# Kernel tuning notes

Measured on AMD Instinct MI355X. Metric: run time of the kernel, lower is better.

## Reference

```python
import jax, jax.numpy as jnp
import numpy as np

DIM = 1024
NUM_HEADS = 16
HEAD_DIM = DIM // NUM_HEADS
SCALE = 1.0 / float(np.sqrt(HEAD_DIM))


def setup_inputs() -> dict:
    key = jax.random.key(0)
    ks = jax.random.split(key, 8)
    b, n = 1, 4096
    x = jax.random.normal(ks[0], (b, n, DIM), dtype=jnp.float32)
    cos = jax.random.uniform(ks[1], (b, n, HEAD_DIM // 2), dtype=jnp.float32)
    sin = jax.random.uniform(ks[2], (b, n, HEAD_DIM // 2), dtype=jnp.float32)
    # qkv Linear(dim, 3*dim) and proj Linear(dim, dim); store weights as [in, out]
    w_qkv = jax.random.normal(ks[3], (DIM, 3 * DIM), dtype=jnp.float32) * (1.0 / np.sqrt(DIM))
    b_qkv = jax.random.normal(ks[4], (3 * DIM,), dtype=jnp.float32) * 0.01
    w_proj = jax.random.normal(ks[5], (DIM, DIM), dtype=jnp.float32) * (1.0 / np.sqrt(DIM))
    b_proj = jax.random.normal(ks[6], (DIM,), dtype=jnp.float32) * 0.01
    return {"x": x, "cos": cos, "sin": sin, "w_qkv": w_qkv, "b_qkv": b_qkv,
            "w_proj": w_proj, "b_proj": b_proj}


def _rotate_half(t):
    t1, t2 = jnp.split(t, 2, axis=-1)
    return jnp.concatenate([-t2, t1], axis=-1)


def reference(x, cos, sin, w_qkv, b_qkv, w_proj, b_proj):
    b, n, d = x.shape
    qkv = x @ w_qkv + b_qkv                      # [b, n, 3d]
    q, k, v = jnp.split(qkv, 3, axis=-1)
    # [b, n, h, hd] layout (avoids explicit transposes; einsum handles head axis)
    q = q.reshape(b, n, NUM_HEADS, HEAD_DIM)
    k = k.reshape(b, n, NUM_HEADS, HEAD_DIM)
    v = v.reshape(b, n, NUM_HEADS, HEAD_DIM)
    # RoPE: cos/sin [b, n, hd/2] -> [b, n, 1, hd], broadcast over heads
    cos_f = jnp.concatenate([cos, cos], axis=-1)[:, :, None, :]
    sin_f = jnp.concatenate([sin, sin], axis=-1)[:, :, None, :]
    q = q * cos_f + _rotate_half(q) * sin_f
    k = k * cos_f + _rotate_half(k) * sin_f
    # SDPA (non-causal, no dropout in eval)
    scores = jnp.einsum("bqhd,bkhd->bhqk", q, k) * SCALE
    attn = jax.nn.softmax(scores, axis=-1)
    out = jnp.einsum("bhqk,bkhd->bqhd", attn, v).reshape(b, n, d)
    return out @ w_proj + b_proj
```

## Files before the change

kernel.cpp:

```cpp
#include <hip/hip_runtime.h>
#include <hip/hip_bf16.h>
#include <cstdint>


#define TOK 4096
#define DIM_ 1024
#define NHEAD 16
#define HDIM 64
#define N3 3072
#define SCALE_LOG2E 0.18033688011112042f

typedef __bf16 bf16_t;
typedef bf16_t bf16x8 __attribute__((ext_vector_type(8)));
typedef float floatx4 __attribute__((ext_vector_type(4)));

__device__ __forceinline__ void async_ld16(const bf16_t* g, bf16_t* l) {
  __builtin_amdgcn_global_load_lds(
      (const __attribute__((address_space(1))) void*)(g),
      (__attribute__((address_space(3))) void*)(l), 16, 0, 0);
}

__global__ __launch_bounds__(256) void k_prep(
    const float* __restrict__ x, const float* __restrict__ w_qkv,
    const float* __restrict__ w_proj, bf16_t* __restrict__ xb,
    bf16_t* __restrict__ wqkvT, bf16_t* __restrict__ wprojT) {
  __shared__ float tile[32][33];
  const int b = blockIdx.x;
  if (b < 4096) {
    int i = b * 256 + threadIdx.x;
    float4 v = ((const float4*)x)[i];
    union { bf16_t bb[4]; uint64_t u; } p;
    p.bb[0] = (bf16_t)v.x; p.bb[1] = (bf16_t)v.y;
    p.bb[2] = (bf16_t)v.z; p.bb[3] = (bf16_t)v.w;
    ((uint64_t*)xb)[i] = p.u;
    return;
  }
  const float* in; bf16_t* out; int R, C, c0, r0;
  if (b < 7168) {
    int bb = b - 4096; in = w_qkv; out = wqkvT; R = 1024; C = 3072;
    c0 = (bb % 96) * 32; r0 = (bb / 96) * 32;
  } else {
    int bb = b - 7168; in = w_proj; out = wprojT; R = 1024; C = 1024;
    c0 = (bb % 32) * 32; r0 = (bb / 32) * 32;
  }
  int tx = threadIdx.x & 31, ty = threadIdx.x >> 5;
#pragma unroll
  for (int i = 0; i < 4; i++) {
    int r = ty + i * 8;
    tile[r][tx] = in[(size_t)(r0 + r) * C + c0 + tx];
  }
  __syncthreads();
#pragma unroll
  for (int i = 0; i < 4; i++) {
    int c = ty + i * 8;
    out[(size_t)(c0 + c) * R + r0 + tx] = (bf16_t)tile[tx][c];
  }
}

__global__ __launch_bounds__(256) void k_qkv(
    const bf16_t* __restrict__ A,
    const bf16_t* __restrict__ Bt,
    const float* __restrict__ bias,
    const float* __restrict__ cs,
    const float* __restrict__ sn,
    bf16_t* __restrict__ qb, bf16_t* __restrict__ kb, bf16_t* __restrict__ vT) {
  constexpr int K = 1024, BK = 32;
  __shared__ bf16_t As[128 * BK] __attribute__((aligned(16)));
  __shared__ bf16_t Bs[128 * BK] __attribute__((aligned(16)));
  const int t = threadIdx.x;
  const int lane = t & 63, w = t >> 6;
  const int lrow = lane & 15, quad = lane >> 4;
  const int m0 = blockIdx.y * 128, n0 = blockIdx.x * 128;
  const int wm = (w >> 1) * 64, wn = (w & 1) * 64;

  const floatx4 ZV = {0.f, 0.f, 0.f, 0.f};
  floatx4 acc[4][4];
#pragma unroll
  for (int i = 0; i < 4; i++)
#pragma unroll
    for (int j = 0; j < 4; j++) acc[i][j] = ZV;

  for (int kt = 0; kt < K; kt += BK) {
#pragma unroll
    for (int r = 0; r < 2; r++) {
      int idx = r * 256 + t;
      int lbase = (r * 256 + w * 64) * 8;
      async_ld16(&A[(size_t)(m0 + (idx >> 2)) * K + kt + (idx & 3) * 8], &As[lbase]);
      async_ld16(&Bt[(size_t)(n0 + (idx >> 2)) * K + kt + (idx & 3) * 8], &Bs[lbase]);
    }
    __syncthreads();
    bf16x8 af[4], bf[4];
#pragma unroll
    for (int i = 0; i < 4; i++)
      af[i] = *(const bf16x8*)&As[(wm + i * 16 + lrow) * BK + quad * 8];
#pragma unroll
    for (int i = 0; i < 4; i++)
      bf[i] = *(const bf16x8*)&Bs[(wn + i * 16 + lrow) * BK + quad * 8];
#pragma unroll
    for (int mi = 0; mi < 4; mi++)
#pragma unroll
      for (int ni = 0; ni < 4; ni++)
        acc[mi][ni] = __builtin_amdgcn_mfma_f32_16x16x32_bf16(af[mi], bf[ni], acc[mi][ni], 0, 0, 0);
    __syncthreads();
  }

  const int c0 = n0 + wn;
  const int seg = c0 >> 10;
  const int h = (c0 & 1023) >> 6;
  float bv[4];
#pragma unroll
  for (int ni = 0; ni < 4; ni++) bv[ni] = bias[c0 + ni * 16 + lrow];

  if (seg < 2) {
    bf16_t* base = ((seg == 0) ? qb : kb) + (size_t)h * TOK * HDIM;
    const float qs = (seg == 0) ? SCALE_LOG2E : 1.0f;
#pragma unroll
    for (int mi = 0; mi < 4; mi++) {
#pragma unroll
      for (int reg = 0; reg < 4; reg++) {
        const int r = m0 + wm + mi * 16 + quad * 4 + reg;
        const float c_lo = cs[r * 32 + lrow];
        const float c_hi = cs[r * 32 + 16 + lrow];
        const float s_lo = sn[r * 32 + lrow];
        const float s_hi = sn[r * 32 + 16 + lrow];
        const float v0 = acc[mi][0][reg] + bv[0];
        const float v1 = acc[mi][1][reg] + bv[1];
        const float v2 = acc[mi][2][reg] + bv[2];
        const float v3 = acc[mi][3][reg] + bv[3];
        const float o0 = (v0 * c_lo - v2 * s_lo) * qs;
        const float o1 = (v1 * c_hi - v3 * s_hi) * qs;
        const float o2 = (v2 * c_lo + v0 * s_lo) * qs;
        const float o3 = (v3 * c_hi + v1 * s_hi) * qs;
        bf16_t* rp = base + (size_t)r * HDIM + lrow;
        rp[0]  = (bf16_t)o0;
        rp[16] = (bf16_t)o1;
        rp[32] = (bf16_t)o2;
        rp[48] = (bf16_t)o3;
      }
    }
  } else {
    bf16_t* base = vT + (size_t)h * HDIM * TOK;
#pragma unroll
    for (int mi = 0; mi < 4; mi++) {
      const int rbase = m0 + wm + mi * 16 + quad * 4;
#pragma unroll
      for (int ni = 0; ni < 4; ni++) {
        union { bf16_t b[4]; uint64_t u; } p;
#pragma unroll
        for (int reg = 0; reg < 4; reg++) p.b[reg] = (bf16_t)(acc[mi][ni][reg] + bv[ni]);
        *(uint64_t*)&base[(size_t)(ni * 16 + lrow) * TOK + rbase] = p.u;
      }
    }
  }
}

__global__ __launch_bounds__(256, 2) void k_attn(
    const bf16_t* __restrict__ qb, const bf16_t* __restrict__ kb,
    const bf16_t* __restrict__ vT, bf16_t* __restrict__ ao) {
  __shared__ bf16_t Ks[2][64 * 64] __attribute__((aligned(16)));
  __shared__ bf16_t Vs[2][64 * 64] __attribute__((aligned(16)));
  __shared__ bf16_t Ps[4][64 * 36] __attribute__((aligned(16)));
  const int t = threadIdx.x, lane = t & 63, w = t >> 6;
  const int lrow = lane & 15, quad = lane >> 4;
  const int qg = w & 1, kh = w >> 1;
  const int h = blockIdx.x & 15;
  const int q0 = (blockIdx.x >> 4) * 128;
  const bf16_t* qh = qb + (size_t)h * TOK * HDIM;
  const bf16_t* khp = kb + (size_t)h * TOK * HDIM;
  const bf16_t* vhp = vT + (size_t)h * HDIM * TOK;
  bf16_t* Pw = &Ps[w][0];

  const int ksrc = (t >> 3) * HDIM + (((t & 7) ^ ((t >> 3) & 7)) * 8);
  const int vsrc = (t >> 3) * TOK + (((t & 7) ^ ((t >> 3) & 7)) * 8);

  bf16x8 qf[4][2];
#pragma unroll
  for (int ni = 0; ni < 4; ni++)
#pragma unroll
    for (int ks = 0; ks < 2; ks++)
      qf[ni][ks] = *(const bf16x8*)&qh[(size_t)(q0 + qg * 64 + ni * 16 + lrow) * HDIM + ks * 32 + quad * 8];

  const floatx4 ZV = {0.f, 0.f, 0.f, 0.f};
  floatx4 o[4][4];
  floatx4 lacc[4] = {ZV, ZV, ZV, ZV};
#pragma unroll
  for (int d = 0; d < 4; d++)
#pragma unroll
    for (int ni = 0; ni < 4; ni++) o[d][ni] = ZV;

#pragma unroll
  for (int r = 0; r < 2; r++) {
    async_ld16(&khp[(size_t)(r * 32) * HDIM + ksrc], &Ks[0][r * 2048 + t * 8]);
    async_ld16(&vhp[(size_t)(r * 32) * TOK + vsrc], &Vs[0][r * 2048 + t * 8]);
  }

  for (int it = 0; it < TOK / 64; ++it) {
    const int b = it & 1;
    __syncthreads();
    if (it + 1 < TOK / 64) {
      const int j1 = (it + 1) * 64;
#pragma unroll
      for (int r = 0; r < 2; r++) {
        async_ld16(&khp[((size_t)j1 + r * 32) * HDIM + ksrc], &Ks[b ^ 1][r * 2048 + t * 8]);
        async_ld16(&vhp[(size_t)(r * 32) * TOK + j1 + vsrc], &Vs[b ^ 1][r * 2048 + t * 8]);
      }
    }

    floatx4 s[2][4];
#pragma unroll
    for (int mi = 0; mi < 2; mi++)
#pragma unroll
      for (int ni = 0; ni < 4; ni++) s[mi][ni] = ZV;
#pragma unroll
    for (int ks = 0; ks < 2; ks++)
#pragma unroll
      for (int mi = 0; mi < 2; mi++) {
        bf16x8 kf = *(const bf16x8*)&Ks[b][(kh * 32 + mi * 16 + lrow) * 64 + (((ks * 4 + quad) ^ (lrow & 7)) * 8)];
#pragma unroll
        for (int ni = 0; ni < 4; ni++)
          s[mi][ni] = __builtin_amdgcn_mfma_f32_16x16x32_bf16(kf, qf[ni][ks], s[mi][ni], 0, 0, 0);
      }

#pragma unroll
    for (int mi = 0; mi < 2; mi++)
#pragma unroll
      for (int ni = 0; ni < 4; ni++) {
#pragma unroll
        for (int reg = 0; reg < 4; reg++)
          s[mi][ni][reg] = __builtin_amdgcn_exp2f(s[mi][ni][reg]);
        lacc[ni] += s[mi][ni];
      }

#pragma unroll
    for (int mi = 0; mi < 2; mi++)
#pragma unroll
      for (int ni = 0; ni < 4; ni++) {
        union { bf16_t b4[4]; uint64_t u; } p;
#pragma unroll
        for (int reg = 0; reg < 4; reg++) p.b4[reg] = (bf16_t)s[mi][ni][reg];
        *(uint64_t*)&Pw[(ni * 16 + lrow) * 36 + (mi * 4 + quad) * 4] = p.u;
      }

    bf16x8 pf[4];
#pragma unroll
    for (int ni = 0; ni < 4; ni++) {
      const int row = (ni * 16 + lrow) * 36;
      union { uint64_t u[2]; bf16x8 v; } pp;
      pp.u[0] = *(const uint64_t*)&Pw[row + quad * 8];
      pp.u[1] = *(const uint64_t*)&Pw[row + quad * 8 + 4];
      pf[ni] = pp.v;
    }
#pragma unroll
    for (int dt = 0; dt < 4; dt++) {
      bf16x8 vf = *(const bf16x8*)&Vs[b][(dt * 16 + lrow) * 64 + (((kh * 4 + quad) ^ (lrow & 7)) * 8)];
#pragma unroll
      for (int ni = 0; ni < 4; ni++)
        o[dt][ni] = __builtin_amdgcn_mfma_f32_16x16x32_bf16(vf, pf[ni], o[dt][ni], 0, 0, 0);
    }
  }

  __syncthreads();
  float* Mrg = (qg == 0) ? (float*)&Ks[0][0] : (float*)&Vs[0][0];
  float* Lmrg = (float*)&Ps[0][0];
  float lq[4];
#pragma unroll
  for (int ni = 0; ni < 4; ni++) {
    float l = lacc[ni][0] + lacc[ni][1] + lacc[ni][2] + lacc[ni][3];
    l += __shfl_xor(l, 16, 64);
    l += __shfl_xor(l, 32, 64);
    lq[ni] = l;
  }
  if (kh == 1) {
#pragma unroll
    for (int ni = 0; ni < 4; ni++) {
#pragma unroll
      for (int dt = 0; dt < 4; dt++)
        *(floatx4*)&Mrg[(ni * 16 + lrow) * 64 + dt * 16 + quad * 4] = o[dt][ni];
      if (quad == 0) Lmrg[qg * 64 + ni * 16 + lrow] = lq[ni];
    }
  }
  __syncthreads();
  if (kh == 0) {
#pragma unroll
    for (int ni = 0; ni < 4; ni++) {
      const float l = lq[ni] + Lmrg[qg * 64 + ni * 16 + lrow];
      const float inv = 1.0f / l;
      const int qrow = q0 + qg * 64 + ni * 16 + lrow;
#pragma unroll
      for (int dt = 0; dt < 4; dt++) {
        floatx4 ov = *(const floatx4*)&Mrg[(ni * 16 + lrow) * 64 + dt * 16 + quad * 4];
        union { bf16_t b4[4]; uint64_t u; } p;
#pragma unroll
        for (int reg = 0; reg < 4; reg++) p.b4[reg] = (bf16_t)((o[dt][ni][reg] + ov[reg]) * inv);
        *(uint64_t*)&ao[(size_t)qrow * DIM_ + h * HDIM + dt * 16 + quad * 4] = p.u;
      }
    }
  }
}

__global__ __launch_bounds__(256) void k_proj(
    const bf16_t* __restrict__ A,
    const bf16_t* __restrict__ Bt,
    const float* __restrict__ bias, float* __restrict__ out) {
  constexpr int K = 1024, BK = 32;
  __shared__ bf16_t As[64 * BK] __attribute__((aligned(16)));
  __shared__ bf16_t Bs[128 * BK] __attribute__((aligned(16)));
  const int t = threadIdx.x;
  const int lane = t & 63, w = t >> 6;
  const int lrow = lane & 15, quad = lane >> 4;
  const int m0 = blockIdx.y * 64, n0 = blockIdx.x * 128;
  const int wm = (w >> 1) * 32, wn = (w & 1) * 64;

  const floatx4 ZV = {0.f, 0.f, 0.f, 0.f};
  floatx4 acc[2][4];
#pragma unroll
  for (int i = 0; i < 2; i++)
#pragma unroll
    for (int j = 0; j < 4; j++) acc[i][j] = ZV;

  for (int kt = 0; kt < K; kt += BK) {
    async_ld16(&A[(size_t)(m0 + (t >> 2)) * K + kt + (t & 3) * 8], &As[w * 512]);
#pragma unroll
    for (int r = 0; r < 2; r++) {
      int idx = r * 256 + t;
      async_ld16(&Bt[(size_t)(n0 + (idx >> 2)) * K + kt + (idx & 3) * 8],
                 &Bs[(r * 256 + w * 64) * 8]);
    }
    __syncthreads();
    bf16x8 af[2], bf[4];
#pragma unroll
    for (int i = 0; i < 2; i++)
      af[i] = *(const bf16x8*)&As[(wm + i * 16 + lrow) * BK + quad * 8];
#pragma unroll
    for (int i = 0; i < 4; i++)
      bf[i] = *(const bf16x8*)&Bs[(wn + i * 16 + lrow) * BK + quad * 8];
#pragma unroll
    for (int mi = 0; mi < 2; mi++)
#pragma unroll
      for (int ni = 0; ni < 4; ni++)
        acc[mi][ni] = __builtin_amdgcn_mfma_f32_16x16x32_bf16(af[mi], bf[ni], acc[mi][ni], 0, 0, 0);
    __syncthreads();
  }

  const int c0 = n0 + wn;
#pragma unroll
  for (int ni = 0; ni < 4; ni++) {
    float bv = bias[c0 + ni * 16 + lrow];
#pragma unroll
    for (int mi = 0; mi < 2; mi++)
#pragma unroll
      for (int reg = 0; reg < 4; reg++) {
        int r = m0 + wm + mi * 16 + quad * 4 + reg;
        out[(size_t)r * DIM_ + c0 + ni * 16 + lrow] = acc[mi][ni][reg] + bv;
      }
  }
}

extern "C" void kernel_launch(void* const* d_in, const int* in_sizes, int n_in,
                              void* d_out, int out_size, void* d_ws, size_t ws_size,
                              hipStream_t stream) {
  const float* x      = (const float*)d_in[0];
  const float* cs     = (const float*)d_in[1];
  const float* sn     = (const float*)d_in[2];
  const float* w_qkv  = (const float*)d_in[3];
  const float* b_qkv  = (const float*)d_in[4];
  const float* w_proj = (const float*)d_in[5];
  const float* b_proj = (const float*)d_in[6];
  float* out = (float*)d_out;

  char* ws = (char*)d_ws;
  bf16_t* xb     = (bf16_t*)(ws);
  bf16_t* wqkvT  = (bf16_t*)(ws + 8388608);
  bf16_t* wprojT = (bf16_t*)(ws + 14680064);
  bf16_t* qb     = (bf16_t*)(ws + 16777216);
  bf16_t* kb     = (bf16_t*)(ws + 25165824);
  bf16_t* vT     = (bf16_t*)(ws + 33554432);
  bf16_t* ao     = xb;

  k_prep<<<dim3(8192), dim3(256), 0, stream>>>(x, w_qkv, w_proj, xb, wqkvT, wprojT);
  k_qkv<<<dim3(24, 32), dim3(256), 0, stream>>>(xb, wqkvT, b_qkv, cs, sn, qb, kb, vT);
  k_attn<<<dim3(512), dim3(256), 0, stream>>>(qb, kb, vT, ao);
  k_proj<<<dim3(8, 64), dim3(256), 0, stream>>>(ao, wprojT, b_proj, out);
}
```

Before: 222.2 us.

## Switch attention to 32x32x16 MFMA and keep P in registers

The attention kernel now uses 32x32x16 bf16 MFMAs instead of 16x16x32. The S accumulator layout then lines up with the B-operand layout the PV MFMA needs, so the exponentiated P tile is packed to bf16 in registers and the per-wave LDS round trip through Ps is dropped. V fragments are read from LDS as two 8-byte halves matching the permuted key order, and the final merge keeps only a small Lm array. This removes LDS traffic and LDS footprint, at the cost of larger accumulators (floatx16) and possible register pressure under launch_bounds(256,2).

Result: slower. 232.4 us (+4.6%).

```diff
diff --git a/kernel.cpp b/kernel.cpp
--- a/kernel.cpp
+++ b/kernel.cpp
@@ -13,11 +13,18 @@
 typedef __bf16 bf16_t;
 typedef bf16_t bf16x8 __attribute__((ext_vector_type(8)));
 typedef float floatx4 __attribute__((ext_vector_type(4)));
+typedef float floatx16 __attribute__((ext_vector_type(16)));
 
 __device__ __forceinline__ void async_ld16(const bf16_t* g, bf16_t* l) {
   __builtin_amdgcn_global_load_lds(
       (const __attribute__((address_space(1))) void*)(g),
       (__attribute__((address_space(3))) void*)(l), 16, 0, 0);
+}
+
+__device__ __forceinline__ uint32_t pkbf(float a, float b) {
+  union { bf16_t h[2]; uint32_t u; } x;
+  x.h[0] = (bf16_t)a; x.h[1] = (bf16_t)b;
+  return x.u;
 }
 
 __global__ __launch_bounds__(256) void k_prep(
@@ -159,34 +166,35 @@
     const bf16_t* __restrict__ vT, bf16_t* __restrict__ ao) {
   __shared__ bf16_t Ks[2][64 * 64] __attribute__((aligned(16)));
   __shared__ bf16_t Vs[2][64 * 64] __attribute__((aligned(16)));
-  __shared__ bf16_t Ps[4][64 * 36] __attribute__((aligned(16)));
+  __shared__ float Lm[128];
   const int t = threadIdx.x, lane = t & 63, w = t >> 6;
-  const int lrow = lane & 15, quad = lane >> 4;
+  const int c32 = lane & 31, h32 = lane >> 5;
   const int qg = w & 1, kh = w >> 1;
   const int h = blockIdx.x & 15;
   const int q0 = (blockIdx.x >> 4) * 128;
   const bf16_t* qh = qb + (size_t)h * TOK * HDIM;
   const bf16_t* khp = kb + (size_t)h * TOK * HDIM;
   const bf16_t* vhp = vT + (size_t)h * HDIM * TOK;
-  bf16_t* Pw = &Ps[w][0];
 
   const int ksrc = (t >> 3) * HDIM + (((t & 7) ^ ((t >> 3) & 7)) * 8);
   const int vsrc = (t >> 3) * TOK + (((t & 7) ^ ((t >> 3) & 7)) * 8);
 
-  bf16x8 qf[4][2];
-#pragma unroll
-  for (int ni = 0; ni < 4; ni++)
-#pragma unroll
-    for (int ks = 0; ks < 2; ks++)
-      qf[ni][ks] = *(const bf16x8*)&qh[(size_t)(q0 + qg * 64 + ni * 16 + lrow) * HDIM + ks * 32 + quad * 8];
-
-  const floatx4 ZV = {0.f, 0.f, 0.f, 0.f};
-  floatx4 o[4][4];
-  floatx4 lacc[4] = {ZV, ZV, ZV, ZV};
-#pragma unroll
-  for (int d = 0; d < 4; d++)
-#pragma unroll
-    for (int ni = 0; ni < 4; ni++) o[d][ni] = ZV;
+  bf16x8 qf[2][4];
+#pragma unroll
+  for (int qt = 0; qt < 2; qt++)
+#pragma unroll
+    for (int ks = 0; ks < 4; ks++)
+      qf[qt][ks] = *(const bf16x8*)&qh[(size_t)(q0 + qg * 64 + qt * 32 + c32) * HDIM + ks * 16 + h32 * 8];
+
+  const floatx4 ZV4 = {0.f, 0.f, 0.f, 0.f};
+  floatx16 o[2][2];
+  floatx4 lacc[2] = {ZV4, ZV4};
+#pragma unroll
+  for (int dt = 0; dt < 2; dt++)
+#pragma unroll
+    for (int qt = 0; qt < 2; qt++)
+#pragma unroll
+      for (int i = 0; i < 16; i++) o[dt][qt][i] = 0.f;
 
 #pragma unroll
   for (int r = 0; r < 2; r++) {
@@ -206,94 +214,94 @@
       }
     }
 
-    floatx4 s[2][4];
-#pragma unroll
-    for (int mi = 0; mi < 2; mi++)
-#pragma unroll
-      for (int ni = 0; ni < 4; ni++) s[mi][ni] = ZV;
-#pragma unroll
-    for (int ks = 0; ks < 2; ks++)
-#pragma unroll
-      for (int mi = 0; mi < 2; mi++) {
-        bf16x8 kf = *(const bf16x8*)&Ks[b][(kh * 32 + mi * 16 + lrow) * 64 + (((ks * 4 + quad) ^ (lrow & 7)) * 8)];
-#pragma unroll
-        for (int ni = 0; ni < 4; ni++)
-          s[mi][ni] = __builtin_amdgcn_mfma_f32_16x16x32_bf16(kf, qf[ni][ks], s[mi][ni], 0, 0, 0);
-      }
-
-#pragma unroll
-    for (int mi = 0; mi < 2; mi++)
-#pragma unroll
-      for (int ni = 0; ni < 4; ni++) {
-#pragma unroll
-        for (int reg = 0; reg < 4; reg++)
-          s[mi][ni][reg] = __builtin_amdgcn_exp2f(s[mi][ni][reg]);
-        lacc[ni] += s[mi][ni];
-      }
-
-#pragma unroll
-    for (int mi = 0; mi < 2; mi++)
-#pragma unroll
-      for (int ni = 0; ni < 4; ni++) {
-        union { bf16_t b4[4]; uint64_t u; } p;
-#pragma unroll
-        for (int reg = 0; reg < 4; reg++) p.b4[reg] = (bf16_t)s[mi][ni][reg];
-        *(uint64_t*)&Pw[(ni * 16 + lrow) * 36 + (mi * 4 + quad) * 4] = p.u;
-      }
-
-    bf16x8 pf[4];
-#pragma unroll
-    for (int ni = 0; ni < 4; ni++) {
-      const int row = (ni * 16 + lrow) * 36;
-      union { uint64_t u[2]; bf16x8 v; } pp;
-      pp.u[0] = *(const uint64_t*)&Pw[row + quad * 8];
-      pp.u[1] = *(const uint64_t*)&Pw[row + quad * 8 + 4];
-      pf[ni] = pp.v;
-    }
-#pragma unroll
-    for (int dt = 0; dt < 4; dt++) {
-      bf16x8 vf = *(const bf16x8*)&Vs[b][(dt * 16 + lrow) * 64 + (((kh * 4 + quad) ^ (lrow & 7)) * 8)];
-#pragma unroll
-      for (int ni = 0; ni < 4; ni++)
-        o[dt][ni] = __builtin_amdgcn_mfma_f32_16x16x32_bf16(vf, pf[ni], o[dt][ni], 0, 0, 0);
-    }
-  }
-
+    floatx16 s[2];
+#pragma unroll
+    for (int i = 0; i < 16; i++) { s[0][i] = 0.f; s[1][i] = 0.f; }
+#pragma unroll
+    for (int ks = 0; ks < 4; ks++) {
+      bf16x8 kf = *(const bf16x8*)&Ks[b][(kh * 32 + c32) * 64 + (((ks * 2 + h32) ^ (c32 & 7)) * 8)];
+#pragma unroll
+      for (int qt = 0; qt < 2; qt++)
+        s[qt] = __builtin_amdgcn_mfma_f32_32x32x16_bf16(kf, qf[qt][ks], s[qt], 0, 0, 0);
+    }
+
+    uint32_t pk[2][8];
+#pragma unroll
+    for (int qt = 0; qt < 2; qt++) {
+#pragma unroll
+      for (int i = 0; i < 16; i++) s[qt][i] = __builtin_amdgcn_exp2f(s[qt][i]);
+#pragma unroll
+      for (int i = 0; i < 4; i++)
+#pragma unroll
+        for (int r = 0; r < 4; r++) lacc[qt][r] += s[qt][i * 4 + r];
+#pragma unroll
+      for (int i = 0; i < 8; i++) pk[qt][i] = pkbf(s[qt][2 * i], s[qt][2 * i + 1]);
+    }
+
+#pragma unroll
+    for (int st = 0; st < 2; st++) {
+      bf16x8 pf[2];
+#pragma unroll
+      for (int qt = 0; qt < 2; qt++) {
+        union { uint32_t u[4]; bf16x8 v; } pp;
+#pragma unroll
+        for (int a = 0; a < 4; a++) pp.u[a] = pk[qt][st * 4 + a];
+        pf[qt] = pp.v;
+      }
+      const int cb = kh * 4 + st * 2;
+#pragma unroll
+      for (int dt = 0; dt < 2; dt++) {
+        const int drow = (dt * 32 + c32) * 64;
+        union { uint64_t u[2]; bf16x8 v; } vv;
+        vv.u[0] = *(const uint64_t*)&Vs[b][drow + ((cb ^ (c32 & 7)) * 8) + 4 * h32];
+        vv.u[1] = *(const uint64_t*)&Vs[b][drow + (((cb + 1) ^ (c32 & 7)) * 8) + 4 * h32];
+#pragma unroll
+        for (int qt = 0; qt < 2; qt++)
+          o[dt][qt] = __builtin_amdgcn_mfma_f32_32x32x16_bf16(vv.v, pf[qt], o[dt][qt], 0, 0, 0);
+      }
+    }
+  }
+
+  float lq[2];
+#pragma unroll
+  for (int qt = 0; qt < 2; qt++) {
+    float l = lacc[qt][0] + lacc[qt][1] + lacc[qt][2] + lacc[qt][3];
+    l += __shfl_xor(l, 32, 64);
+    lq[qt] = l;
+  }
   __syncthreads();
   float* Mrg = (qg == 0) ? (float*)&Ks[0][0] : (float*)&Vs[0][0];
-  float* Lmrg = (float*)&Ps[0][0];
-  float lq[4];
-#pragma unroll
-  for (int ni = 0; ni < 4; ni++) {
-    float l = lacc[ni][0] + lacc[ni][1] + lacc[ni][2] + lacc[ni][3];
-    l += __shfl_xor(l, 16, 64);
-    l += __shfl_xor(l, 32, 64);
-    lq[ni] = l;
-  }
   if (kh == 1) {
 #pragma unroll
-    for (int ni = 0; ni < 4; ni++) {
-#pragma unroll
-      for (int dt = 0; dt < 4; dt++)
-        *(floatx4*)&Mrg[(ni * 16 + lrow) * 64 + dt * 16 + quad * 4] = o[dt][ni];
-      if (quad == 0) Lmrg[qg * 64 + ni * 16 + lrow] = lq[ni];
+    for (int qt = 0; qt < 2; qt++) {
+#pragma unroll
+      for (int dt = 0; dt < 2; dt++)
+#pragma unroll
+        for (int r = 0; r < 4; r++) {
+          floatx4 ov = {o[dt][qt][4 * r], o[dt][qt][4 * r + 1],
+                        o[dt][qt][4 * r + 2], o[dt][qt][4 * r + 3]};
+          *(floatx4*)&Mrg[(qt * 32 + c32) * 64 + dt * 32 + 8 * r + 4 * h32] = ov;
+        }
+      if (h32 == 0) Lm[qg * 64 + qt * 32 + c32] = lq[qt];
     }
   }
   __syncthreads();
   if (kh == 0) {
 #pragma unroll
-    for (int ni = 0; ni < 4; ni++) {
-      const float l = lq[ni] + Lmrg[qg * 64 + ni * 16 + lrow];
-      const float inv = 1.0f / l;
-      const int qrow = q0 + qg * 64 + ni * 16 + lrow;
-#pragma unroll
-      for (int dt = 0; dt < 4; dt++) {
-        floatx4 ov = *(const floatx4*)&Mrg[(ni * 16 + lrow) * 64 + dt * 16 + quad * 4];
-        union { bf16_t b4[4]; uint64_t u; } p;
-#pragma unroll
-        for (int reg = 0; reg < 4; reg++) p.b4[reg] = (bf16_t)((o[dt][ni][reg] + ov[reg]) * inv);
-        *(uint64_t*)&ao[(size_t)qrow * DIM_ + h * HDIM + dt * 16 + quad * 4] = p.u;
-      }
+    for (int qt = 0; qt < 2; qt++) {
+      const float inv = 1.0f / (lq[qt] + Lm[qg * 64 + qt * 32 + c32]);
+      const int qrow = q0 + qg * 64 + qt * 32 + c32;
+#pragma unroll
+      for (int dt = 0; dt < 2; dt++)
+#pragma unroll
+        for (int r = 0; r < 4; r++) {
+          floatx4 ov = *(const floatx4*)&Mrg[(qt * 32 + c32) * 64 + dt * 32 + 8 * r + 4 * h32];
+          union { bf16_t b4[4]; uint64_t u; } p;
+#pragma unroll
+          for (int e = 0; e < 4; e++)
+            p.b4[e] = (bf16_t)((o[dt][qt][4 * r + e] + ov[e]) * inv);
+          *(uint64_t*)&ao[(size_t)qrow * DIM_ + h * HDIM + dt * 32 + 8 * r + 4 * h32] = p.u;
+        }
     }
   }
 }
```
